# Kernel tuning notes

Hardware: AMD Instinct MI355X
Metric: run time of the kernel (lower is better)

Reference implementation:

```python
import jax, jax.numpy as jnp
import numpy as np

DIM = 1024
NUM_SKILLS = 50


def setup_inputs() -> dict:
    key = jax.random.key(0)
    ks = jax.random.split(key, 7)
    n_tokens = 4096
    scale = 1.0 / np.sqrt(DIM)
    x = jax.random.normal(ks[0], (n_tokens, DIM), dtype=jnp.float32)
    # Stacked expert weights: skill i is Linear(dim,dim) -> ReLU -> Linear(dim,dim)
    W1 = jax.random.uniform(ks[1], (NUM_SKILLS, DIM, DIM), jnp.float32, -scale, scale)
    b1 = jax.random.uniform(ks[2], (NUM_SKILLS, DIM), jnp.float32, -scale, scale)
    W2 = jax.random.uniform(ks[3], (NUM_SKILLS, DIM, DIM), jnp.float32, -scale, scale)
    b2 = jax.random.uniform(ks[4], (NUM_SKILLS, DIM), jnp.float32, -scale, scale)
    # Gating linear: Linear(dim, num_skills)
    Wg = jax.random.uniform(ks[5], (DIM, NUM_SKILLS), jnp.float32, -scale, scale)
    bg = jax.random.uniform(ks[6], (NUM_SKILLS,), jnp.float32, -scale, scale)
    return {"x": x, "W1": W1, "b1": b1, "W2": W2, "b2": b2, "Wg": Wg, "bg": bg}


def reference(x, W1, b1, W2, b2, Wg, bg):
    # Soft-MoE path (skill_id=None): softmax gate over all experts,
    # every expert applied to every token, weighted sum.
    gates = jax.nn.softmax(x @ Wg + bg, axis=-1)            # [n, E]
    h = jax.nn.relu(jnp.einsum('nd,edh->neh', x, W1) + b1)  # [n, E, d]
    y = jnp.einsum('neh,ehd->ned', h, W2) + b2              # [n, E, d]
    out = jnp.einsum('ned,ne->nd', y, gates)                # [n, d]
    return out
```

## Files before the change

kernel.cpp:

```cpp
#include <hip/hip_runtime.h>
#include <stdint.h>

#define AS1 __attribute__((address_space(1)))
#define AS3 __attribute__((address_space(3)))

typedef unsigned short u16;
typedef __attribute__((ext_vector_type(8))) short s16x8;
typedef __attribute__((ext_vector_type(8))) unsigned short u16x8;
typedef __attribute__((ext_vector_type(4))) float f32x4;

__device__ __forceinline__ u16 f2bf(float f) {
    union { float f; unsigned int u; } v; v.f = f;
    unsigned int r = v.u + 0x7fffu + ((v.u >> 16) & 1u);
    return (u16)(r >> 16);
}

__device__ __forceinline__ void gld_lds16(const u16* g, u16* l) {
    __builtin_amdgcn_global_load_lds((AS1 unsigned int*)(uintptr_t)g,
                                     (AS3 unsigned int*)(uintptr_t)l, 16, 0, 0);
}

__global__ void convert_x_kernel(const float* __restrict__ X, u16* __restrict__ Xb, int total8) {
    int i = blockIdx.x * 256 + threadIdx.x;
    if (i < total8) {
        f32x4 a = ((const f32x4*)X)[2 * i];
        f32x4 b = ((const f32x4*)X)[2 * i + 1];
        u16x8 o;
#pragma unroll
        for (int j = 0; j < 4; j++) { o[j] = f2bf(a[j]); o[4 + j] = f2bf(b[j]); }
        ((u16x8*)Xb)[i] = o;
    }
}

__global__ void gate_kernel(const float* __restrict__ X, const float* __restrict__ Wg,
                            const float* __restrict__ bg, float* __restrict__ gates, int nt) {
    __shared__ float xs[1024];
    const int n = blockIdx.x;
    const int t = threadIdx.x;
#pragma unroll
    for (int i = 0; i < 16; i++) xs[t + i * 64] = X[(size_t)n * 1024 + t + i * 64];
    __syncthreads();
    float a = -INFINITY;
    if (t < 50) {
        float s0 = 0.f, s1 = 0.f, s2 = 0.f, s3 = 0.f;
        for (int d = 0; d < 1024; d += 4) {
            s0 += xs[d + 0] * Wg[(d + 0) * 50 + t];
            s1 += xs[d + 1] * Wg[(d + 1) * 50 + t];
            s2 += xs[d + 2] * Wg[(d + 2) * 50 + t];
            s3 += xs[d + 3] * Wg[(d + 3) * 50 + t];
        }
        a = (s0 + s1) + (s2 + s3) + bg[t];
    }
    float m = a;
#pragma unroll
    for (int off = 32; off > 0; off >>= 1) m = fmaxf(m, __shfl_xor(m, off));
    float p = (t < 50) ? __expf(a - m) : 0.f;
    float ss = p;
#pragma unroll
    for (int off = 32; off > 0; off >>= 1) ss += __shfl_xor(ss, off);
    if (t < 50) gates[(size_t)n * 50 + t] = p / ss;
}

__global__ void transpose_kernel(const float* __restrict__ W1s, const float* __restrict__ W2s,
                                 u16* __restrict__ Wt1, u16* __restrict__ Wt2, int eg) {
    __shared__ u16 tile[64 * 65];
    const int t = threadIdx.x;
    const int z = blockIdx.z;
    const float* src; u16* dst;
    if (z < eg) { src = W1s + ((size_t)z << 20); dst = Wt1 + ((size_t)z << 20); }
    else        { src = W2s + ((size_t)(z - eg) << 20); dst = Wt2 + ((size_t)(z - eg) << 20); }
    const int k0 = blockIdx.y * 64;
    const int n0 = blockIdx.x * 64;
#pragma unroll
    for (int p = 0; p < 4; p++) {
        int r = (t >> 4) + 16 * p;
        int c = t & 15;
        f32x4 v = *(const f32x4*)(src + (size_t)(k0 + r) * 1024 + n0 + c * 4);
#pragma unroll
        for (int j = 0; j < 4; j++) tile[r * 65 + c * 4 + j] = f2bf(v[j]);
    }
    __syncthreads();
#pragma unroll
    for (int p = 0; p < 2; p++) {
        int h = (t >> 3) + 32 * p;
        int c = t & 7;
        u16x8 o;
#pragma unroll
        for (int j = 0; j < 8; j++) o[j] = tile[(c * 8 + j) * 65 + h];
        *(u16x8*)(dst + (size_t)(n0 + h) * 1024 + k0 + c * 8) = o;
    }
}


#define BUF_U16 16384

#define STG1(t) { int bo = ((t) & 3) * BUF_U16;                                   \
        const u16* a = Ag + (t) * 32; const u16* b = Bg + (t) * 32;               \
        gld_lds16(a, Ald + bo);          gld_lds16(a + 131072, Ald + bo + 4096);  \
        gld_lds16(b, Bld + bo);          gld_lds16(b + 131072, Bld + bo + 4096); }

#define STG2(t) { int kt = kb + (t) * 32; int ee = kt >> 10; int kk = kt & 1023;  \
        const u16* a = Agr + (size_t)ee * ntk + kk;                               \
        const u16* b = Bgr + ((size_t)ee << 20) + kk;                             \
        int bo = ((t) & 3) * BUF_U16;                                             \
        gld_lds16(a, Ald + bo);          gld_lds16(a + 131072, Ald + bo + 4096);  \
        gld_lds16(b, Bld + bo);          gld_lds16(b + 131072, Bld + bo + 4096); }

#define MMSTEP(t, VM, DO, STG) {                                                  \
        asm volatile("s_waitcnt vmcnt(" VM ")\n\ts_barrier" ::: "memory");        \
        if (DO) STG((t) + 3);                                                     \
        const u16* bp = smem + ((t) & 3) * BUF_U16;                               \
        s16x8 av[8], bv[4];                                                       \
        _Pragma("unroll") for (int mi = 0; mi < 8; mi++)                          \
            av[mi] = *(const s16x8*)(bp + aoff[mi]);                              \
        _Pragma("unroll") for (int nj = 0; nj < 4; nj++)                          \
            bv[nj] = *(const s16x8*)(bp + boff[nj]);                              \
        __builtin_amdgcn_s_setprio(1);                                            \
        _Pragma("unroll") for (int mi = 0; mi < 8; mi++)                          \
        _Pragma("unroll") for (int nj = 0; nj < 4; nj++)                          \
            acc[mi * 4 + nj] = __builtin_amdgcn_mfma_f32_16x16x32_bf16(           \
                av[mi], bv[nj], acc[mi * 4 + nj], 0, 0, 0);                       \
        __builtin_amdgcn_s_setprio(0); }

__global__ __launch_bounds__(512, 2)
void gemm1_kernel(const u16* __restrict__ X, const u16* __restrict__ Wt1,
                  const float* __restrict__ b1, const float* __restrict__ gates,
                  u16* __restrict__ Hp, int nt, int egbase) {
    __shared__ __align__(16) u16 smem[67584];
    const int tid = threadIdx.x, wave = tid >> 6, lane = tid & 63;
    const int e = blockIdx.z;
    const int n0 = blockIdx.x * 256, m0 = blockIdx.y * 256;

    const int srow = wave * 16 + (lane >> 2);
    const int scg = ((lane & 3) ^ ((srow >> 1) & 3)) * 8;
    const u16* Ag = X + (size_t)(m0 + srow) * 1024 + scg;
    const u16* Bg = Wt1 + ((size_t)e << 20) + (size_t)(n0 + srow) * 1024 + scg;
    u16* Ald = smem + wave * 512;
    u16* Bld = smem + 8192 + wave * 512;

    const int wm = wave >> 2, wn = wave & 3;
    const int fr = lane & 15, fq = lane >> 4;
    int aoff[8], boff[4];
#pragma unroll
    for (int mi = 0; mi < 8; mi++) {
        int ra = wm * 128 + mi * 16 + fr;
        aoff[mi] = ra * 32 + ((fq ^ ((ra >> 1) & 3)) * 8);
    }
#pragma unroll
    for (int nj = 0; nj < 4; nj++) {
        int rb = wn * 64 + nj * 16 + fr;
        boff[nj] = 8192 + rb * 32 + ((fq ^ ((rb >> 1) & 3)) * 8);
    }

    f32x4 acc[32];
#pragma unroll
    for (int i = 0; i < 32; i++) acc[i] = (f32x4){0.f, 0.f, 0.f, 0.f};

    STG1(0); STG1(1); STG1(2);
    for (int t = 0; t < 29; ++t) MMSTEP(t, "8", 1, STG1);
    MMSTEP(29, "8", 0, STG1);
    MMSTEP(30, "4", 0, STG1);
    MMSTEP(31, "0", 0, STG1);

    const float* b1e = b1 + (size_t)e * 1024;
    float b1v[4];
#pragma unroll
    for (int nj = 0; nj < 4; nj++) b1v[nj] = b1e[n0 + wn * 64 + nj * 16 + fr];
    const int eglob = egbase + e;

    __syncthreads();
#pragma unroll
    for (int mi = 0; mi < 8; mi++) {
#pragma unroll
        for (int ri = 0; ri < 4; ri++) {
            int row = wm * 128 + mi * 16 + fq * 4 + ri;
            float g = gates[(size_t)(m0 + row) * 50 + eglob];
#pragma unroll
            for (int nj = 0; nj < 4; nj++) {
                int col = wn * 64 + nj * 16 + fr;
                float h = acc[mi * 4 + nj][ri] + b1v[nj];
                h = h > 0.f ? h * g : 0.f;
                smem[row * 264 + col] = f2bf(h);
            }
        }
    }
    __syncthreads();
    u16* HpE = Hp + (size_t)e * nt * 1024;
    const int c = tid & 31, rr = tid >> 5;
#pragma unroll
    for (int p = 0; p < 16; p++) {
        int r = rr + p * 16;
        u16x8 v = *(const u16x8*)(smem + r * 264 + c * 8);
        *(u16x8*)(HpE + (size_t)(m0 + r) * 1024 + n0 + c * 8) = v;
    }
}

__global__ __launch_bounds__(512, 2)
void gemm2_kernel(const u16* __restrict__ Hp, const u16* __restrict__ Wt2,
                  float* __restrict__ partial, int nt, int eg, int init) {
    __shared__ __align__(16) u16 smem[65536];
    const int tid = threadIdx.x, wave = tid >> 6, lane = tid & 63;
    const int s = blockIdx.z;
    const int n0 = blockIdx.x * 256, m0 = blockIdx.y * 256;

    const int srow = wave * 16 + (lane >> 2);
    const int scg = ((lane & 3) ^ ((srow >> 1) & 3)) * 8;
    const u16* Agr = Hp + (size_t)(m0 + srow) * 1024 + scg;
    const u16* Bgr = Wt2 + (size_t)(n0 + srow) * 1024 + scg;
    const size_t ntk = (size_t)nt * 1024;
    u16* Ald = smem + wave * 512;
    u16* Bld = smem + 8192 + wave * 512;

    const int wm = wave >> 2, wn = wave & 3;
    const int fr = lane & 15, fq = lane >> 4;
    int aoff[8], boff[4];
#pragma unroll
    for (int mi = 0; mi < 8; mi++) {
        int ra = wm * 128 + mi * 16 + fr;
        aoff[mi] = ra * 32 + ((fq ^ ((ra >> 1) & 3)) * 8);
    }
#pragma unroll
    for (int nj = 0; nj < 4; nj++) {
        int rb = wn * 64 + nj * 16 + fr;
        boff[nj] = 8192 + rb * 32 + ((fq ^ ((rb >> 1) & 3)) * 8);
    }

    f32x4 acc[32];
#pragma unroll
    for (int i = 0; i < 32; i++) acc[i] = (f32x4){0.f, 0.f, 0.f, 0.f};

    const int NT = eg * 8;
    const int kb = s * NT * 32;

    STG2(0); STG2(1); STG2(2);
    for (int t = 0; t < NT - 3; ++t) MMSTEP(t, "8", 1, STG2);
    MMSTEP(NT - 3, "8", 0, STG2);
    MMSTEP(NT - 2, "4", 0, STG2);
    MMSTEP(NT - 1, "0", 0, STG2);

    float* pp = partial + (size_t)s * nt * 1024;
#pragma unroll
    for (int mi = 0; mi < 8; mi++) {
#pragma unroll
        for (int ri = 0; ri < 4; ri++) {
            int gr = m0 + wm * 128 + mi * 16 + fq * 4 + ri;
#pragma unroll
            for (int nj = 0; nj < 4; nj++) {
                size_t idx = (size_t)gr * 1024 + n0 + wn * 64 + nj * 16 + fr;
                float v = acc[mi * 4 + nj][ri];
                if (!init) v += pp[idx];
                pp[idx] = v;
            }
        }
    }
}

__global__ void finalize_kernel(const float* __restrict__ partial, const float* __restrict__ gates,
                                const float* __restrict__ b2, float* __restrict__ out, int nt) {
    __shared__ float gs[50];
    const int n = blockIdx.x;
    const int t = threadIdx.x;
    if (t < 50) gs[t] = gates[(size_t)n * 50 + t];
    __syncthreads();
    const size_t base = (size_t)n * 1024;
    const size_t st = (size_t)nt * 1024;
#pragma unroll
    for (int i = 0; i < 4; i++) {
        int d = t + i * 256;
        float v = partial[base + d] + partial[st + base + d]
                + partial[2 * st + base + d] + partial[3 * st + base + d];
#pragma unroll 10
        for (int e2 = 0; e2 < 50; e2++) v += gs[e2] * b2[e2 * 1024 + d];
        out[base + d] = v;
    }
}

extern "C" void kernel_launch(void* const* d_in, const int* in_sizes, int n_in,
                              void* d_out, int out_size, void* d_ws, size_t ws_size,
                              hipStream_t stream) {
    const float* x  = (const float*)d_in[0];
    const float* W1 = (const float*)d_in[1];
    const float* b1 = (const float*)d_in[2];
    const float* W2 = (const float*)d_in[3];
    const float* b2 = (const float*)d_in[4];
    const float* Wg = (const float*)d_in[5];
    const float* bg = (const float*)d_in[6];
    float* out = (float*)d_out;
    const int nt = in_sizes[0] / 1024;

    char* w = (char*)d_ws;
    auto carve = [&](size_t bytes) -> char* {
        char* p = w; w += (bytes + 255) & ~(size_t)255; return p;
    };
    float* gates   = (float*)carve((size_t)nt * 50 * 4);
    float* partial = (float*)carve((size_t)4 * nt * 1024 * 4);
    u16*   xb      = (u16*)carve((size_t)nt * 1024 * 2);
    const size_t fixed = (size_t)(w - (char*)d_ws);

    int eg = 1;
    const int cand[6] = {50, 25, 10, 5, 2, 1};
    for (int i = 0; i < 6; i++) {
        size_t need = fixed + (size_t)cand[i] * ((size_t)2 * 2097152 + (size_t)nt * 1024 * 2) + 4096;
        if (need <= ws_size) { eg = cand[i]; break; }
    }
    u16* Wt1 = (u16*)carve((size_t)eg * 1048576 * 2);
    u16* Wt2 = (u16*)carve((size_t)eg * 1048576 * 2);
    u16* Hp  = (u16*)carve((size_t)eg * nt * 1024 * 2);

    convert_x_kernel<<<(nt * 1024 / 8 + 255) / 256, 256, 0, stream>>>(x, xb, nt * 1024 / 8);
    gate_kernel<<<nt, 64, 0, stream>>>(x, Wg, bg, gates, nt);

    const int groups = 50 / eg;
    for (int g = 0; g < groups; ++g) {
        transpose_kernel<<<dim3(16, 16, 2 * eg), 256, 0, stream>>>(
            W1 + ((size_t)(g * eg) << 20), W2 + ((size_t)(g * eg) << 20), Wt1, Wt2, eg);
        gemm1_kernel<<<dim3(4, nt / 256, eg), 512, 0, stream>>>(
            xb, Wt1, b1 + (size_t)g * eg * 1024, gates, Hp, nt, g * eg);
        gemm2_kernel<<<dim3(4, nt / 256, 4), 512, 0, stream>>>(
            Hp, Wt2, partial, nt, eg, g == 0 ? 1 : 0);
    }
    finalize_kernel<<<nt, 256, 0, stream>>>(partial, gates, b2, out, nt);
}
```

Baseline: 1.389 ms.

## Shrink GEMM block tiles to 128x256 with 4 waves and triple buffering

Both expert GEMM kernels go from 512-thread blocks with 256x256 output tiles and a 4-stage LDS ring to 256-thread blocks with 128x256 tiles and a 3-stage ring. The grid is reordered so the token dimension is blockIdx.x. Smaller blocks and LDS use are meant to raise occupancy and scheduling flexibility. In exchange, each block reuses the B tile over fewer rows, so there is more global traffic per FLOP, and the prefetch depth is shallower.

```diff
diff --git a/kernel.cpp b/kernel.cpp
--- a/kernel.cpp
+++ b/kernel.cpp
@@ -92,24 +92,32 @@
 }
 
 
-#define BUF_U16 16384
-
-#define STG1(t) { int bo = ((t) & 3) * BUF_U16;                                   \
+#define BUF_U16 12288
+
+#define STG1(t) { int bo = ((t) % 3) * BUF_U16;                                   \
         const u16* a = Ag + (t) * 32; const u16* b = Bg + (t) * 32;               \
-        gld_lds16(a, Ald + bo);          gld_lds16(a + 131072, Ald + bo + 4096);  \
-        gld_lds16(b, Bld + bo);          gld_lds16(b + 131072, Bld + bo + 4096); }
+        gld_lds16(a,          Al + bo);                                           \
+        gld_lds16(a + 65536,  Al + bo + 2048);                                    \
+        gld_lds16(b,          Bl + bo);                                           \
+        gld_lds16(b + 65536,  Bl + bo + 2048);                                    \
+        gld_lds16(b + 131072, Bl + bo + 4096);                                    \
+        gld_lds16(b + 196608, Bl + bo + 6144); }
 
 #define STG2(t) { int kt = kb + (t) * 32; int ee = kt >> 10; int kk = kt & 1023;  \
         const u16* a = Agr + (size_t)ee * ntk + kk;                               \
         const u16* b = Bgr + ((size_t)ee << 20) + kk;                             \
-        int bo = ((t) & 3) * BUF_U16;                                             \
-        gld_lds16(a, Ald + bo);          gld_lds16(a + 131072, Ald + bo + 4096);  \
-        gld_lds16(b, Bld + bo);          gld_lds16(b + 131072, Bld + bo + 4096); }
+        int bo = ((t) % 3) * BUF_U16;                                             \
+        gld_lds16(a,          Al + bo);                                           \
+        gld_lds16(a + 65536,  Al + bo + 2048);                                    \
+        gld_lds16(b,          Bl + bo);                                           \
+        gld_lds16(b + 65536,  Bl + bo + 2048);                                    \
+        gld_lds16(b + 131072, Bl + bo + 4096);                                    \
+        gld_lds16(b + 196608, Bl + bo + 6144); }
 
 #define MMSTEP(t, VM, DO, STG) {                                                  \
         asm volatile("s_waitcnt vmcnt(" VM ")\n\ts_barrier" ::: "memory");        \
-        if (DO) STG((t) + 3);                                                     \
-        const u16* bp = smem + ((t) & 3) * BUF_U16;                               \
+        if (DO) STG((t) + 2);                                                     \
+        const u16* bp = smem + ((t) % 3) * BUF_U16;                               \
         s16x8 av[8], bv[4];                                                       \
         _Pragma("unroll") for (int mi = 0; mi < 8; mi++)                          \
             av[mi] = *(const s16x8*)(bp + aoff[mi]);                              \
@@ -122,50 +130,48 @@
                 av[mi], bv[nj], acc[mi * 4 + nj], 0, 0, 0);                       \
         __builtin_amdgcn_s_setprio(0); }
 
-__global__ __launch_bounds__(512, 2)
+__global__ __launch_bounds__(256, 2)
 void gemm1_kernel(const u16* __restrict__ X, const u16* __restrict__ Wt1,
                   const float* __restrict__ b1, const float* __restrict__ gates,
                   u16* __restrict__ Hp, int nt, int egbase) {
-    __shared__ __align__(16) u16 smem[67584];
+    __shared__ __align__(16) u16 smem[36864];
     const int tid = threadIdx.x, wave = tid >> 6, lane = tid & 63;
     const int e = blockIdx.z;
-    const int n0 = blockIdx.x * 256, m0 = blockIdx.y * 256;
+    const int m0 = blockIdx.x * 128, n0 = blockIdx.y * 256;
 
     const int srow = wave * 16 + (lane >> 2);
     const int scg = ((lane & 3) ^ ((srow >> 1) & 3)) * 8;
     const u16* Ag = X + (size_t)(m0 + srow) * 1024 + scg;
     const u16* Bg = Wt1 + ((size_t)e << 20) + (size_t)(n0 + srow) * 1024 + scg;
-    u16* Ald = smem + wave * 512;
-    u16* Bld = smem + 8192 + wave * 512;
-
-    const int wm = wave >> 2, wn = wave & 3;
+    u16* Al = smem + wave * 512;
+    u16* Bl = smem + 4096 + wave * 512;
+
     const int fr = lane & 15, fq = lane >> 4;
     int aoff[8], boff[4];
 #pragma unroll
     for (int mi = 0; mi < 8; mi++) {
-        int ra = wm * 128 + mi * 16 + fr;
+        int ra = mi * 16 + fr;
         aoff[mi] = ra * 32 + ((fq ^ ((ra >> 1) & 3)) * 8);
     }
 #pragma unroll
     for (int nj = 0; nj < 4; nj++) {
-        int rb = wn * 64 + nj * 16 + fr;
-        boff[nj] = 8192 + rb * 32 + ((fq ^ ((rb >> 1) & 3)) * 8);
+        int rb = wave * 64 + nj * 16 + fr;
+        boff[nj] = 4096 + rb * 32 + ((fq ^ ((rb >> 1) & 3)) * 8);
     }
 
     f32x4 acc[32];
 #pragma unroll
     for (int i = 0; i < 32; i++) acc[i] = (f32x4){0.f, 0.f, 0.f, 0.f};
 
-    STG1(0); STG1(1); STG1(2);
-    for (int t = 0; t < 29; ++t) MMSTEP(t, "8", 1, STG1);
-    MMSTEP(29, "8", 0, STG1);
-    MMSTEP(30, "4", 0, STG1);
+    STG1(0); STG1(1);
+    for (int t = 0; t < 30; ++t) MMSTEP(t, "6", 1, STG1);
+    MMSTEP(30, "6", 0, STG1);
     MMSTEP(31, "0", 0, STG1);
 
     const float* b1e = b1 + (size_t)e * 1024;
     float b1v[4];
 #pragma unroll
-    for (int nj = 0; nj < 4; nj++) b1v[nj] = b1e[n0 + wn * 64 + nj * 16 + fr];
+    for (int nj = 0; nj < 4; nj++) b1v[nj] = b1e[n0 + wave * 64 + nj * 16 + fr];
     const int eglob = egbase + e;
 
     __syncthreads();
@@ -173,11 +179,11 @@
     for (int mi = 0; mi < 8; mi++) {
 #pragma unroll
         for (int ri = 0; ri < 4; ri++) {
-            int row = wm * 128 + mi * 16 + fq * 4 + ri;
+            int row = mi * 16 + fq * 4 + ri;
             float g = gates[(size_t)(m0 + row) * 50 + eglob];
 #pragma unroll
             for (int nj = 0; nj < 4; nj++) {
-                int col = wn * 64 + nj * 16 + fr;
+                int col = wave * 64 + nj * 16 + fr;
                 float h = acc[mi * 4 + nj][ri] + b1v[nj];
                 h = h > 0.f ? h * g : 0.f;
                 smem[row * 264 + col] = f2bf(h);
@@ -189,40 +195,39 @@
     const int c = tid & 31, rr = tid >> 5;
 #pragma unroll
     for (int p = 0; p < 16; p++) {
-        int r = rr + p * 16;
+        int r = rr + p * 8;
         u16x8 v = *(const u16x8*)(smem + r * 264 + c * 8);
         *(u16x8*)(HpE + (size_t)(m0 + r) * 1024 + n0 + c * 8) = v;
     }
 }
 
-__global__ __launch_bounds__(512, 2)
+__global__ __launch_bounds__(256, 2)
 void gemm2_kernel(const u16* __restrict__ Hp, const u16* __restrict__ Wt2,
                   float* __restrict__ partial, int nt, int eg, int init) {
-    __shared__ __align__(16) u16 smem[65536];
+    __shared__ __align__(16) u16 smem[36864];
     const int tid = threadIdx.x, wave = tid >> 6, lane = tid & 63;
     const int s = blockIdx.z;
-    const int n0 = blockIdx.x * 256, m0 = blockIdx.y * 256;
+    const int m0 = blockIdx.x * 128, n0 = blockIdx.y * 256;
 
     const int srow = wave * 16 + (lane >> 2);
     const int scg = ((lane & 3) ^ ((srow >> 1) & 3)) * 8;
     const u16* Agr = Hp + (size_t)(m0 + srow) * 1024 + scg;
     const u16* Bgr = Wt2 + (size_t)(n0 + srow) * 1024 + scg;
     const size_t ntk = (size_t)nt * 1024;
-    u16* Ald = smem + wave * 512;
-    u16* Bld = smem + 8192 + wave * 512;
-
-    const int wm = wave >> 2, wn = wave & 3;
+    u16* Al = smem + wave * 512;
+    u16* Bl = smem + 4096 + wave * 512;
+
     const int fr = lane & 15, fq = lane >> 4;
     int aoff[8], boff[4];
 #pragma unroll
     for (int mi = 0; mi < 8; mi++) {
-        int ra = wm * 128 + mi * 16 + fr;
+        int ra = mi * 16 + fr;
         aoff[mi] = ra * 32 + ((fq ^ ((ra >> 1) & 3)) * 8);
     }
 #pragma unroll
     for (int nj = 0; nj < 4; nj++) {
-        int rb = wn * 64 + nj * 16 + fr;
-        boff[nj] = 8192 + rb * 32 + ((fq ^ ((rb >> 1) & 3)) * 8);
+        int rb = wave * 64 + nj * 16 + fr;
+        boff[nj] = 4096 + rb * 32 + ((fq ^ ((rb >> 1) & 3)) * 8);
     }
 
     f32x4 acc[32];
@@ -232,10 +237,9 @@
     const int NT = eg * 8;
     const int kb = s * NT * 32;
 
-    STG2(0); STG2(1); STG2(2);
-    for (int t = 0; t < NT - 3; ++t) MMSTEP(t, "8", 1, STG2);
-    MMSTEP(NT - 3, "8", 0, STG2);
-    MMSTEP(NT - 2, "4", 0, STG2);
+    STG2(0); STG2(1);
+    for (int t = 0; t < NT - 2; ++t) MMSTEP(t, "6", 1, STG2);
+    MMSTEP(NT - 2, "6", 0, STG2);
     MMSTEP(NT - 1, "0", 0, STG2);
 
     float* pp = partial + (size_t)s * nt * 1024;
@@ -243,10 +247,10 @@
     for (int mi = 0; mi < 8; mi++) {
 #pragma unroll
         for (int ri = 0; ri < 4; ri++) {
-            int gr = m0 + wm * 128 + mi * 16 + fq * 4 + ri;
+            int gr = m0 + mi * 16 + fq * 4 + ri;
 #pragma unroll
             for (int nj = 0; nj < 4; nj++) {
-                size_t idx = (size_t)gr * 1024 + n0 + wn * 64 + nj * 16 + fr;
+                size_t idx = (size_t)gr * 1024 + n0 + wave * 64 + nj * 16 + fr;
                 float v = acc[mi * 4 + nj][ri];
                 if (!init) v += pp[idx];
                 pp[idx] = v;
@@ -314,9 +318,9 @@
     for (int g = 0; g < groups; ++g) {
         transpose_kernel<<<dim3(16, 16, 2 * eg), 256, 0, stream>>>(
             W1 + ((size_t)(g * eg) << 20), W2 + ((size_t)(g * eg) << 20), Wt1, Wt2, eg);
-        gemm1_kernel<<<dim3(4, nt / 256, eg), 512, 0, stream>>>(
+        gemm1_kernel<<<dim3(nt / 128, 4, eg), 256, 0, stream>>>(
             xb, Wt1, b1 + (size_t)g * eg * 1024, gates, Hp, nt, g * eg);
-        gemm2_kernel<<<dim3(4, nt / 256, 4), 512, 0, stream>>>(
+        gemm2_kernel<<<dim3(nt / 128, 4, 4), 256, 0, stream>>>(
             Hp, Wt2, partial, nt, eg, g == 0 ? 1 : 0);
     }
     finalize_kernel<<<nt, 256, 0, stream>>>(partial, gates, b2, out, nt);
```

Result: slower. 1.427 ms (+2.7%).
